# Kernel tuning notes

Measured on AMD Instinct MI355X. Metric: run time of the kernel, lower is better.

The kernel has to match this reference:

```python
import jax, jax.numpy as jnp
import numpy as np

N_STEPS = 128
DT = 0.001
TAU_M = 10.0 * DT            # NeuroTorch LIFLayer default tau_m = 10*dt
ALPHA = float(np.exp(-DT / TAU_M))
THRESHOLD = 1.0
GAMMA = 100.0                # surrogate-gradient sharpness

@jax.custom_vjp
def spike_fn(v):
    # Heaviside spike with sigmoid surrogate gradient (HeavisideSigmoidApprox)
    return (v >= THRESHOLD).astype(v.dtype)

def _spike_fwd(v):
    return spike_fn(v), v

def _spike_bwd(v, g):
    s = jax.nn.sigmoid(GAMMA * (v - THRESHOLD))
    return (g * GAMMA * s * (1.0 - s),)

spike_fn.defvjp(_spike_fwd, _spike_bwd)

def setup_inputs() -> dict:
    key = jax.random.key(0)
    B, N = 256, 2048
    x = jax.random.normal(key, (B, N), dtype=jnp.float32)
    W = jnp.eye(N, dtype=jnp.float32)  # default forward_weights = eye(n_units)
    return {"x": x, "W": W}

def reference(x, W):
    B, N = x.shape
    # ConstantValuesTransform repeats x over all n_steps, so the input current
    # I = x @ W is identical every step; hoist it out of the scan.
    I = x @ W  # [B, N]
    V0 = jnp.zeros((B, N), dtype=x.dtype)
    Z0 = jnp.zeros((B, N), dtype=x.dtype)

    def step(carry, _):
        V, Z = carry
        # reset via previous spikes (detached in original: Z.detach())
        V_next = (ALPHA * V + I) * (1.0 - jax.lax.stop_gradient(Z))
        Z_next = spike_fn(V_next)
        return (V_next, Z_next), Z_next

    _, spikes = jax.lax.scan(step, (V0, Z0), None, length=N_STEPS)  # [T, B, N]
    return jnp.transpose(spikes, (1, 0, 2))  # [B, T, N] like torch.stack(dim=1)
```

## Files before the change

kernel.cpp:

```cpp
#include <hip/hip_runtime.h>
#include <cstddef>

#define Mdim 256
#define Ndim 2048
#define Kdim 2048
#define Tsteps 128

#define MT 128
#define NT 128
#define KT 16

typedef float v4f __attribute__((ext_vector_type(4)));

__global__ __launch_bounds__(256, 2) void gemm_part_kernel(
    const float* __restrict__ x, const float* __restrict__ W,
    float* __restrict__ ws, int KS)
{
    __shared__ float As[KT][MT + 4];
    __shared__ float Bs[KT][NT + 4];

    const int tid = threadIdx.x;
    const int nb = blockIdx.x;
    const int mb = blockIdx.y;
    const int kb = blockIdx.z;
    const int KC = Kdim / KS;
    const int ntiles = KC / KT;
    const int k_begin = kb * KC;
    const int m0 = mb * MT;
    const int n0 = nb * NT;

    const int am = tid >> 1;
    const int ak = (tid & 1) * 8;
    const int bk = tid >> 4;
    const int bn = (tid & 15) * 8;

    const int tn = tid & 15;
    const int tm = tid >> 4;

    const float* xrow = x + (size_t)(m0 + am) * Kdim + k_begin + ak;
    const float* wrow = W + (size_t)(k_begin + bk) * Ndim + n0 + bn;

    float4 av0 = *(const float4*)(xrow);
    float4 av1 = *(const float4*)(xrow + 4);
    float4 bv0 = *(const float4*)(wrow);
    float4 bv1 = *(const float4*)(wrow + 4);

    float acc[8][8];
#pragma unroll
    for (int i = 0; i < 8; ++i)
#pragma unroll
        for (int j = 0; j < 8; ++j) acc[i][j] = 0.0f;

    for (int t = 0; t < ntiles; ++t) {
        if (t > 0) __syncthreads();
        As[ak + 0][am] = av0.x;
        As[ak + 1][am] = av0.y;
        As[ak + 2][am] = av0.z;
        As[ak + 3][am] = av0.w;
        As[ak + 4][am] = av1.x;
        As[ak + 5][am] = av1.y;
        As[ak + 6][am] = av1.z;
        As[ak + 7][am] = av1.w;
        *(float4*)&Bs[bk][bn]     = bv0;
        *(float4*)&Bs[bk][bn + 4] = bv1;
        __syncthreads();

        if (t + 1 < ntiles) {
            const float* xn = xrow + (size_t)(t + 1) * KT;
            const float* wn = wrow + (size_t)(t + 1) * KT * Ndim;
            av0 = *(const float4*)(xn);
            av1 = *(const float4*)(xn + 4);
            bv0 = *(const float4*)(wn);
            bv1 = *(const float4*)(wn + 4);
        }

#pragma unroll 8
        for (int kk = 0; kk < KT; ++kk) {
            const float4 a0 = *(const float4*)&As[kk][tm * 8];
            const float4 a1 = *(const float4*)&As[kk][tm * 8 + 4];
            const float4 b0 = *(const float4*)&Bs[kk][tn * 4];
            const float4 b1 = *(const float4*)&Bs[kk][tn * 4 + 64];
            const float aa[8] = {a0.x, a0.y, a0.z, a0.w, a1.x, a1.y, a1.z, a1.w};
            const float bb[8] = {b0.x, b0.y, b0.z, b0.w, b1.x, b1.y, b1.z, b1.w};
#pragma unroll
            for (int i = 0; i < 8; ++i)
#pragma unroll
                for (int j = 0; j < 8; ++j)
                    acc[i][j] = fmaf(aa[i], bb[j], acc[i][j]);
        }
    }

    float* wsp = ws + (size_t)kb * Mdim * Ndim;
#pragma unroll
    for (int i = 0; i < 8; ++i) {
        const int m = m0 + tm * 8 + i;
        float4 o0 = {acc[i][0], acc[i][1], acc[i][2], acc[i][3]};
        float4 o1 = {acc[i][4], acc[i][5], acc[i][6], acc[i][7]};
        *(float4*)&wsp[(size_t)m * Ndim + n0 + tn * 4]      = o0;
        *(float4*)&wsp[(size_t)m * Ndim + n0 + tn * 4 + 64] = o1;
    }
}

__global__ __launch_bounds__(256) void lif_sim_kernel(
    const float* __restrict__ ws, float* __restrict__ out, int KS)
{
    const int t4  = blockIdx.x * 256 + threadIdx.x;
    const int idx = t4 * 4;
    const int b = idx / Ndim;
    const int n = idx % Ndim;

    float4 I = *(const float4*)&ws[(size_t)b * Ndim + n];
    for (int ks = 1; ks < KS; ++ks) {
        const float4 p = *(const float4*)&ws[(size_t)ks * Mdim * Ndim + (size_t)b * Ndim + n];
        I.x = __fadd_rn(I.x, p.x);
        I.y = __fadd_rn(I.y, p.y);
        I.z = __fadd_rn(I.z, p.z);
        I.w = __fadd_rn(I.w, p.w);
    }
    const float Iv[4] = {I.x, I.y, I.z, I.w};

    const float ALPHA = (float)0.9048374180359595;

    float V[4] = {0.0f, 0.0f, 0.0f, 0.0f};
    float Z[4] = {0.0f, 0.0f, 0.0f, 0.0f};

    float* op = out + (size_t)b * Tsteps * Ndim + n;
#pragma unroll 4
    for (int t = 0; t < Tsteps; ++t) {
#pragma unroll
        for (int j = 0; j < 4; ++j) {
            float v = __fmul_rn(ALPHA, V[j]);
            v = __fadd_rn(v, Iv[j]);
            v = __fmul_rn(v, __fsub_rn(1.0f, Z[j]));
            V[j] = v;
            Z[j] = (v >= 1.0f) ? 1.0f : 0.0f;
        }
        v4f s = {Z[0], Z[1], Z[2], Z[3]};
        __builtin_nontemporal_store(s, (v4f*)&op[(size_t)t * Ndim]);
    }
}

extern "C" void kernel_launch(void* const* d_in, const int* in_sizes, int n_in,
                              void* d_out, int out_size, void* d_ws, size_t ws_size,
                              hipStream_t stream) {
    const float* x = (const float*)d_in[0];
    const float* W = (const float*)d_in[1];
    float* out = (float*)d_out;
    float* ws  = (float*)d_ws;

    const size_t plane = (size_t)Mdim * Ndim * sizeof(float);
    int KS = 1;
    if (ws_size >= 16 * plane)     KS = 16;
    else if (ws_size >= 8 * plane) KS = 8;
    else if (ws_size >= 4 * plane) KS = 4;
    else if (ws_size >= 2 * plane) KS = 2;

    dim3 ggrid(Ndim / NT, Mdim / MT, KS);
    gemm_part_kernel<<<ggrid, 256, 0, stream>>>(x, W, ws, KS);

    const int sim_threads = Mdim * Ndim / 4;
    lif_sim_kernel<<<dim3(sim_threads / 256), 256, 0, stream>>>(ws, out, KS);
}
```

Before: 302.1 us.

## Double-buffer GEMM shared tiles and skip all-zero weight tiles

Shared-memory A/B tiles are double-buffered so the next tile is stored while the current one is consumed, which cuts one barrier per iteration. Each wave also ballots whether its slice of the weight tile is nonzero and writes a per-buffer flag, and the block skips the FMA loop when the whole W tile is zero. With the identity weight matrix most 16x128 tiles of W are zero, so most GEMM arithmetic is meant to be skipped. The skip is exact for any input, but it only pays off for sparse W, and it adds ballot and flag overhead plus twice the shared memory.

```diff
diff --git a/kernel.cpp b/kernel.cpp
--- a/kernel.cpp
+++ b/kernel.cpp
@@ -16,8 +16,9 @@
     const float* __restrict__ x, const float* __restrict__ W,
     float* __restrict__ ws, int KS)
 {
-    __shared__ float As[KT][MT + 4];
-    __shared__ float Bs[KT][NT + 4];
+    __shared__ float As[2][KT][MT + 4];
+    __shared__ float Bs[2][KT][NT + 4];
+    __shared__ int nzf[2][4] __attribute__((aligned(16)));
 
     const int tid = threadIdx.x;
     const int nb = blockIdx.x;
@@ -28,6 +29,7 @@
     const int k_begin = kb * KC;
     const int m0 = mb * MT;
     const int n0 = nb * NT;
+    const int wave = tid >> 6;
 
     const int am = tid >> 1;
     const int ak = (tid & 1) * 8;
@@ -45,6 +47,27 @@
     float4 bv0 = *(const float4*)(wrow);
     float4 bv1 = *(const float4*)(wrow + 4);
 
+    As[0][ak + 0][am] = av0.x;  As[0][ak + 1][am] = av0.y;
+    As[0][ak + 2][am] = av0.z;  As[0][ak + 3][am] = av0.w;
+    As[0][ak + 4][am] = av1.x;  As[0][ak + 5][am] = av1.y;
+    As[0][ak + 6][am] = av1.z;  As[0][ak + 7][am] = av1.w;
+    *(float4*)&Bs[0][bk][bn]     = bv0;
+    *(float4*)&Bs[0][bk][bn + 4] = bv1;
+    {
+        const bool nz = (bv0.x != 0.0f) | (bv0.y != 0.0f) | (bv0.z != 0.0f) |
+                        (bv0.w != 0.0f) | (bv1.x != 0.0f) | (bv1.y != 0.0f) |
+                        (bv1.z != 0.0f) | (bv1.w != 0.0f);
+        const unsigned long long m = __ballot(nz);
+        if ((tid & 63) == 0) nzf[0][wave] = (m != 0ull) ? 1 : 0;
+    }
+    if (1 < ntiles) {
+        av0 = *(const float4*)(xrow + KT);
+        av1 = *(const float4*)(xrow + KT + 4);
+        bv0 = *(const float4*)(wrow + (size_t)KT * Ndim);
+        bv1 = *(const float4*)(wrow + (size_t)KT * Ndim + 4);
+    }
+    __syncthreads();
+
     float acc[8][8];
 #pragma unroll
     for (int i = 0; i < 8; ++i)
@@ -52,42 +75,50 @@
         for (int j = 0; j < 8; ++j) acc[i][j] = 0.0f;
 
     for (int t = 0; t < ntiles; ++t) {
-        if (t > 0) __syncthreads();
-        As[ak + 0][am] = av0.x;
-        As[ak + 1][am] = av0.y;
-        As[ak + 2][am] = av0.z;
-        As[ak + 3][am] = av0.w;
-        As[ak + 4][am] = av1.x;
-        As[ak + 5][am] = av1.y;
-        As[ak + 6][am] = av1.z;
-        As[ak + 7][am] = av1.w;
-        *(float4*)&Bs[bk][bn]     = bv0;
-        *(float4*)&Bs[bk][bn + 4] = bv1;
-        __syncthreads();
+        const int cur = t & 1;
+        const int nxt = cur ^ 1;
 
         if (t + 1 < ntiles) {
-            const float* xn = xrow + (size_t)(t + 1) * KT;
-            const float* wn = wrow + (size_t)(t + 1) * KT * Ndim;
+            As[nxt][ak + 0][am] = av0.x;  As[nxt][ak + 1][am] = av0.y;
+            As[nxt][ak + 2][am] = av0.z;  As[nxt][ak + 3][am] = av0.w;
+            As[nxt][ak + 4][am] = av1.x;  As[nxt][ak + 5][am] = av1.y;
+            As[nxt][ak + 6][am] = av1.z;  As[nxt][ak + 7][am] = av1.w;
+            *(float4*)&Bs[nxt][bk][bn]     = bv0;
+            *(float4*)&Bs[nxt][bk][bn + 4] = bv1;
+            const bool nz = (bv0.x != 0.0f) | (bv0.y != 0.0f) | (bv0.z != 0.0f) |
+                            (bv0.w != 0.0f) | (bv1.x != 0.0f) | (bv1.y != 0.0f) |
+                            (bv1.z != 0.0f) | (bv1.w != 0.0f);
+            const unsigned long long m = __ballot(nz);
+            if ((tid & 63) == 0) nzf[nxt][wave] = (m != 0ull) ? 1 : 0;
+        }
+
+        if (t + 2 < ntiles) {
+            const float* xn = xrow + (size_t)(t + 2) * KT;
+            const float* wn = wrow + (size_t)(t + 2) * KT * Ndim;
             av0 = *(const float4*)(xn);
             av1 = *(const float4*)(xn + 4);
             bv0 = *(const float4*)(wn);
             bv1 = *(const float4*)(wn + 4);
         }
 
+        const int4 f = *(const int4*)&nzf[cur][0];
+        if (f.x | f.y | f.z | f.w) {
 #pragma unroll 8
-        for (int kk = 0; kk < KT; ++kk) {
-            const float4 a0 = *(const float4*)&As[kk][tm * 8];
-            const float4 a1 = *(const float4*)&As[kk][tm * 8 + 4];
-            const float4 b0 = *(const float4*)&Bs[kk][tn * 4];
-            const float4 b1 = *(const float4*)&Bs[kk][tn * 4 + 64];
-            const float aa[8] = {a0.x, a0.y, a0.z, a0.w, a1.x, a1.y, a1.z, a1.w};
-            const float bb[8] = {b0.x, b0.y, b0.z, b0.w, b1.x, b1.y, b1.z, b1.w};
+            for (int kk = 0; kk < KT; ++kk) {
+                const float4 a0 = *(const float4*)&As[cur][kk][tm * 8];
+                const float4 a1 = *(const float4*)&As[cur][kk][tm * 8 + 4];
+                const float4 b0 = *(const float4*)&Bs[cur][kk][tn * 4];
+                const float4 b1 = *(const float4*)&Bs[cur][kk][tn * 4 + 64];
+                const float aa[8] = {a0.x, a0.y, a0.z, a0.w, a1.x, a1.y, a1.z, a1.w};
+                const float bb[8] = {b0.x, b0.y, b0.z, b0.w, b1.x, b1.y, b1.z, b1.w};
 #pragma unroll
-            for (int i = 0; i < 8; ++i)
+                for (int i = 0; i < 8; ++i)
 #pragma unroll
-                for (int j = 0; j < 8; ++j)
-                    acc[i][j] = fmaf(aa[i], bb[j], acc[i][j]);
+                    for (int j = 0; j < 8; ++j)
+                        acc[i][j] = fmaf(aa[i], bb[j], acc[i][j]);
+            }
         }
+        __syncthreads();
     }
 
     float* wsp = ws + (size_t)kb * Mdim * Ndim;
```

New measurement: 293.8 us. 1.03x faster.
